# Optimization experiments

Hardware: AMD Instinct MI355X
Metric: run time of the kernel (lower is better)

The kernel has to match this reference:

```python
import jax, jax.numpy as jnp
import numpy as np

N_USERS = 100000
N_ITEMS = 50000
DIM = 64
NNZ_FULL = 3000000
NNZ_USER = 1500000
NNZ_ITEM = 750000


def setup_inputs() -> dict:
    key = jax.random.key(0)
    ks = jax.random.split(key, 11)
    N = N_USERS + N_ITEMS
    return {
        "user_emb": jax.random.normal(ks[0], (N_USERS, DIM), jnp.float32) * 0.1,
        "item_emb": jax.random.normal(ks[1], (N_ITEMS, DIM), jnp.float32) * 0.1,
        "full_rows": jax.random.randint(ks[2], (NNZ_FULL,), 0, N, jnp.int32),
        "full_cols": jax.random.randint(ks[3], (NNZ_FULL,), 0, N, jnp.int32),
        "full_vals": jax.random.uniform(ks[4], (NNZ_FULL,), jnp.float32),
        "user_rows": jax.random.randint(ks[5], (NNZ_USER,), 0, N_USERS, jnp.int32),
        "user_cols": jax.random.randint(ks[6], (NNZ_USER,), 0, N_USERS, jnp.int32),
        "user_vals": jax.random.uniform(ks[7], (NNZ_USER,), jnp.float32),
        "item_rows": jax.random.randint(ks[8], (NNZ_ITEM,), 0, N_ITEMS, jnp.int32),
        "item_cols": jax.random.randint(ks[9], (NNZ_ITEM,), 0, N_ITEMS, jnp.int32),
        "item_vals": jax.random.uniform(ks[10], (NNZ_ITEM,), jnp.float32),
    }


def _spmm(rows, cols, vals, x, n_rows):
    # COO sparse @ dense: gather columns, scale by edge value, scatter-add to rows.
    return jax.ops.segment_sum(vals[:, None] * x[cols], rows, num_segments=n_rows)


def reference(user_emb, item_emb,
              full_rows, full_cols, full_vals,
              user_rows, user_cols, user_vals,
              item_rows, item_cols, item_vals):
    n_u, n_i = user_emb.shape[0], item_emb.shape[0]
    all_emb = jnp.concatenate([user_emb, item_emb], axis=0)        # [(Nu+Ni), D]
    all_emb1 = _spmm(full_rows, full_cols, full_vals, all_emb, n_u + n_i)
    user_emb2 = _spmm(user_rows, user_cols, user_vals, user_emb, n_u)
    item_emb2 = _spmm(item_rows, item_cols, item_vals, item_emb, n_i)
    user_emb1, item_emb1 = all_emb1[:n_u], all_emb1[n_u:]
    return (user_emb1, item_emb1, user_emb2, item_emb2)
```

## Files before the change

kernel.cpp:

```cpp
#include <hip/hip_runtime.h>

#define NR_FULL 150000
#define NR_USER 100000
#define NR_ITEM 50000
#define NR_TOT  300000
#define NUSR    100000
#define NR_X    150000
#define DIM     64

#define BIN_ROWS  512
#define BIN_SHIFT 9
#define NBIN ((NR_TOT + BIN_ROWS - 1) / BIN_ROWS)

#define PART_E 8192
#define PART_T 512

#define SORT_T    512
#define SORT_CAP  12288
#define SORT2_CAP 5888

typedef __attribute__((ext_vector_type(4))) float f32x4;

__device__ __forceinline__ unsigned short f2bf(float f) {
    unsigned b = __float_as_uint(f);
    return (unsigned short)((b + 0x7fffu + ((b >> 16) & 1u)) >> 16);
}

__global__ void prep_kernel(const float* __restrict__ ue, const float* __restrict__ ie,
                            unsigned short* __restrict__ tbl,
                            const int* __restrict__ fr, int nf,
                            const int* __restrict__ ur, int nu,
                            const int* __restrict__ ir, int ni,
                            int* __restrict__ bincnt) {
    __shared__ int s_h[NBIN];
    for (int b = threadIdx.x; b < NBIN; b += blockDim.x) s_h[b] = 0;
    __syncthreads();

    int t = blockIdx.x * blockDim.x + threadIdx.x;
    int stride = gridDim.x * blockDim.x;

    const int nq = NR_X * (DIM / 4);
    for (int q = t; q < nq; q += stride) {
        int u  = q >> 4;
        int d4 = q & 15;
        const float* src = ((u < NUSR) ? ue + (size_t)u * DIM
                                       : ie + (size_t)(u - NUSR) * DIM) + d4 * 4;
        f32x4 f = *(const f32x4*)src;
        ushort4 h;
        h.x = f2bf(f.x); h.y = f2bf(f.y); h.z = f2bf(f.z); h.w = f2bf(f.w);
        ((ushort4*)tbl)[q] = h;
    }

    int nvec = nf >> 2;
    for (int i = t; i < nvec; i += stride) {
        int4 r4 = ((const int4*)fr)[i];
        atomicAdd(&s_h[r4.x >> BIN_SHIFT], 1);
        atomicAdd(&s_h[r4.y >> BIN_SHIFT], 1);
        atomicAdd(&s_h[r4.z >> BIN_SHIFT], 1);
        atomicAdd(&s_h[r4.w >> BIN_SHIFT], 1);
    }
    for (int i = (nvec << 2) + t; i < nf; i += stride)
        atomicAdd(&s_h[fr[i] >> BIN_SHIFT], 1);

    nvec = nu >> 2;
    for (int i = t; i < nvec; i += stride) {
        int4 r4 = ((const int4*)ur)[i];
        atomicAdd(&s_h[(r4.x + NR_FULL) >> BIN_SHIFT], 1);
        atomicAdd(&s_h[(r4.y + NR_FULL) >> BIN_SHIFT], 1);
        atomicAdd(&s_h[(r4.z + NR_FULL) >> BIN_SHIFT], 1);
        atomicAdd(&s_h[(r4.w + NR_FULL) >> BIN_SHIFT], 1);
    }
    for (int i = (nvec << 2) + t; i < nu; i += stride)
        atomicAdd(&s_h[(ur[i] + NR_FULL) >> BIN_SHIFT], 1);

    nvec = ni >> 2;
    for (int i = t; i < nvec; i += stride) {
        int4 r4 = ((const int4*)ir)[i];
        atomicAdd(&s_h[(r4.x + NR_FULL + NR_USER) >> BIN_SHIFT], 1);
        atomicAdd(&s_h[(r4.y + NR_FULL + NR_USER) >> BIN_SHIFT], 1);
        atomicAdd(&s_h[(r4.z + NR_FULL + NR_USER) >> BIN_SHIFT], 1);
        atomicAdd(&s_h[(r4.w + NR_FULL + NR_USER) >> BIN_SHIFT], 1);
    }
    for (int i = (nvec << 2) + t; i < ni; i += stride)
        atomicAdd(&s_h[(ir[i] + NR_FULL + NR_USER) >> BIN_SHIFT], 1);

    __syncthreads();
    for (int b = threadIdx.x; b < NBIN; b += blockDim.x) {
        int c = s_h[b];
        if (c) atomicAdd(&bincnt[b], c);
    }
}

__global__ void hist_all(const int* __restrict__ fr, int nf,
                         const int* __restrict__ ur, int nu,
                         const int* __restrict__ ir, int ni,
                         int* __restrict__ bincnt) {
    __shared__ int s_h[NBIN];
    for (int b = threadIdx.x; b < NBIN; b += blockDim.x) s_h[b] = 0;
    __syncthreads();
    int t = blockIdx.x * blockDim.x + threadIdx.x;
    int stride = gridDim.x * blockDim.x;
    int nvec = nf >> 2;
    for (int i = t; i < nvec; i += stride) {
        int4 r4 = ((const int4*)fr)[i];
        atomicAdd(&s_h[r4.x >> BIN_SHIFT], 1);
        atomicAdd(&s_h[r4.y >> BIN_SHIFT], 1);
        atomicAdd(&s_h[r4.z >> BIN_SHIFT], 1);
        atomicAdd(&s_h[r4.w >> BIN_SHIFT], 1);
    }
    for (int i = (nvec << 2) + t; i < nf; i += stride)
        atomicAdd(&s_h[fr[i] >> BIN_SHIFT], 1);
    nvec = nu >> 2;
    for (int i = t; i < nvec; i += stride) {
        int4 r4 = ((const int4*)ur)[i];
        atomicAdd(&s_h[(r4.x + NR_FULL) >> BIN_SHIFT], 1);
        atomicAdd(&s_h[(r4.y + NR_FULL) >> BIN_SHIFT], 1);
        atomicAdd(&s_h[(r4.z + NR_FULL) >> BIN_SHIFT], 1);
        atomicAdd(&s_h[(r4.w + NR_FULL) >> BIN_SHIFT], 1);
    }
    for (int i = (nvec << 2) + t; i < nu; i += stride)
        atomicAdd(&s_h[(ur[i] + NR_FULL) >> BIN_SHIFT], 1);
    nvec = ni >> 2;
    for (int i = t; i < nvec; i += stride) {
        int4 r4 = ((const int4*)ir)[i];
        atomicAdd(&s_h[(r4.x + NR_FULL + NR_USER) >> BIN_SHIFT], 1);
        atomicAdd(&s_h[(r4.y + NR_FULL + NR_USER) >> BIN_SHIFT], 1);
        atomicAdd(&s_h[(r4.z + NR_FULL + NR_USER) >> BIN_SHIFT], 1);
        atomicAdd(&s_h[(r4.w + NR_FULL + NR_USER) >> BIN_SHIFT], 1);
    }
    for (int i = (nvec << 2) + t; i < ni; i += stride)
        atomicAdd(&s_h[(ir[i] + NR_FULL + NR_USER) >> BIN_SHIFT], 1);
    __syncthreads();
    for (int b = threadIdx.x; b < NBIN; b += blockDim.x) {
        int c = s_h[b];
        if (c) atomicAdd(&bincnt[b], c);
    }
}

__global__ void bin_scan(const int* __restrict__ bincnt, int* __restrict__ binoff,
                         int* __restrict__ gcursor, int nnz_tot) {
    __shared__ int s[NBIN];
    int t = threadIdx.x;
    if (t < NBIN) s[t] = bincnt[t];
    __syncthreads();
    for (int off = 1; off < NBIN; off <<= 1) {
        int a = 0;
        if (t < NBIN && t >= off) a = s[t - off];
        __syncthreads();
        if (t < NBIN) s[t] += a;
        __syncthreads();
    }
    if (t < NBIN) {
        int excl = (t == 0) ? 0 : s[t - 1];
        binoff[t] = excl;
        gcursor[t] = excl;
    }
    if (t == 0) binoff[NBIN] = nnz_tot;
}

__global__ __launch_bounds__(PART_T) void partition_kernel(
    const int* __restrict__ fr, const int* __restrict__ fc, const float* __restrict__ fv, int nf,
    const int* __restrict__ ur, const int* __restrict__ uc, const float* __restrict__ uv, int nu,
    const int* __restrict__ ir, const int* __restrict__ ic, const float* __restrict__ iv, int ni,
    int* __restrict__ gcursor, long long* __restrict__ pairs) {
    __shared__ long long s_stage[PART_E];
    __shared__ int s_cnt[NBIN];
    __shared__ int s_start[NBIN + 1];
    __shared__ int s_cur[NBIN];
    __shared__ int s_gbase[NBIN];

    const int t = threadIdx.x;
    const int ntot = nf + nu + ni;
    const int base = blockIdx.x * PART_E;
    const int nE = min(PART_E, ntot - base);

    for (int b = t; b < NBIN; b += PART_T) s_cnt[b] = 0;
    __syncthreads();

    for (int k = 0; k < PART_E / PART_T; ++k) {
        int j = k * PART_T + t;
        if (j < nE) {
            int i = base + j;
            int g;
            if (i < nf)            g = fr[i];
            else if (i < nf + nu)  g = ur[i - nf] + NR_FULL;
            else                   g = ir[i - nf - nu] + NR_FULL + NR_USER;
            atomicAdd(&s_cnt[g >> BIN_SHIFT], 1);
        }
    }
    __syncthreads();

    for (int off = 1; off < NBIN; off <<= 1) {
        int i0 = t, i1 = t + PART_T;
        int a0 = (i0 < NBIN && i0 >= off) ? s_cnt[i0 - off] : 0;
        int a1 = (i1 < NBIN && i1 >= off) ? s_cnt[i1 - off] : 0;
        __syncthreads();
        if (i0 < NBIN) s_cnt[i0] += a0;
        if (i1 < NBIN) s_cnt[i1] += a1;
        __syncthreads();
    }
    for (int b = t; b < NBIN; b += PART_T) {
        int st = (b == 0) ? 0 : s_cnt[b - 1];
        s_start[b] = st;
        s_cur[b]   = st;
    }
    if (t == 0) s_start[NBIN] = s_cnt[NBIN - 1];
    __syncthreads();

    for (int b = t; b < NBIN; b += PART_T) {
        int cnt = s_start[b + 1] - s_start[b];
        s_gbase[b] = cnt ? atomicAdd(&gcursor[b], cnt) : 0;
    }

    for (int k = 0; k < PART_E / PART_T; ++k) {
        int j = k * PART_T + t;
        if (j < nE) {
            int i = base + j;
            int g, u; float v;
            if (i < nf)           { g = fr[i];                          u = fc[i];        v = fv[i]; }
            else if (i < nf + nu) { int q = i - nf;      g = ur[q] + NR_FULL;            u = uc[q];        v = uv[q]; }
            else                  { int q = i - nf - nu; g = ir[q] + NR_FULL + NR_USER;  u = ic[q] + NUSR; v = iv[q]; }
            int bin = g >> BIN_SHIFT;
            int rl  = g & (BIN_ROWS - 1);
            int lpos = atomicAdd(&s_cur[bin], 1);
            unsigned hi = ((unsigned)rl << 18) | (unsigned)u;
            s_stage[lpos] = ((long long)hi << 32) | (long long)__float_as_uint(v);
        }
    }
    __syncthreads();

    for (int j = t; j < nE; j += PART_T) {
        int lo = 0, hi2 = NBIN;
        while (hi2 - lo > 1) {
            int mid = (lo + hi2) >> 1;
            if (s_start[mid] <= j) lo = mid; else hi2 = mid;
        }
        pairs[s_gbase[lo] + (j - s_start[lo])] = s_stage[j];
    }
}

__global__ __launch_bounds__(SORT_T) void sort_bins_split(
    const int* __restrict__ binoff, const long long* __restrict__ pairs,
    long long* __restrict__ pairs2, int* __restrict__ rowptr, int nnz_tot) {
    __shared__ long long s_stage[SORT2_CAP];
    __shared__ int s_cnt[BIN_ROWS];
    __shared__ int s_start[BIN_ROWS];
    __shared__ int s_cur[BIN_ROWS];

    const int t    = threadIdx.x;
    const int bin  = blockIdx.x >> 1;
    const int half = blockIdx.x & 1;
    const int r0   = half * (BIN_ROWS / 2);
    const int r1   = r0 + (BIN_ROWS / 2);
    const int beg  = binoff[bin], end = binoff[bin + 1];
    const int nE   = end - beg;

    s_cnt[t] = 0;
    __syncthreads();

    const unsigned* hi32 = (const unsigned*)(pairs + beg) + 1;
    for (int j = t; j < nE; j += SORT_T)
        atomicAdd(&s_cnt[hi32[2 * j] >> 18], 1);
    __syncthreads();

    for (int off = 1; off < BIN_ROWS; off <<= 1) {
        int a = (t >= off) ? s_cnt[t - off] : 0;
        __syncthreads();
        s_cnt[t] += a;
        __syncthreads();
    }
    int excl = (t == 0) ? 0 : s_cnt[t - 1];
    s_start[t] = excl;
    s_cur[t]   = excl;
    if (t >= r0 && t < r1) {
        int g = bin * BIN_ROWS + t;
        if (g < NR_TOT) rowptr[g] = beg + excl;
    }
    if (bin == 0 && half == 0 && t == 0) rowptr[NR_TOT] = nnz_tot;
    __syncthreads();

    const int myBase  = s_start[r0];
    const int myCount = ((r1 < BIN_ROWS) ? s_start[r1] : s_cnt[BIN_ROWS - 1]) - myBase;
    const int nS = myCount < SORT2_CAP ? myCount : SORT2_CAP;

    for (int j = t; j < nE; j += SORT_T) {
        long long pe = pairs[beg + j];
        int rl = (int)((unsigned)((unsigned long long)pe >> 32) >> 18);
        if (rl >= r0 && rl < r1) {
            int pos = atomicAdd(&s_cur[rl], 1) - myBase;
            if (pos < SORT2_CAP) s_stage[pos] = pe;
        }
    }
    __syncthreads();

    for (int j = t; j < nS; j += SORT_T)
        pairs2[beg + myBase + j] = s_stage[j];
}

__global__ __launch_bounds__(SORT_T) void sort_bins(
    const int* __restrict__ binoff, long long* __restrict__ pairs,
    int* __restrict__ rowptr, int nnz_tot) {
    __shared__ long long s_stage[SORT_CAP];
    __shared__ int s_cnt[BIN_ROWS];
    __shared__ int s_start[BIN_ROWS];
    __shared__ int s_cur[BIN_ROWS];

    const int t   = threadIdx.x;
    const int bin = blockIdx.x;
    const int beg = binoff[bin], end = binoff[bin + 1];
    const int nE  = end - beg;
    const int nS  = nE < SORT_CAP ? nE : SORT_CAP;

    s_cnt[t] = 0;
    __syncthreads();
    for (int j = t; j < nE; j += SORT_T) {
        unsigned hi = (unsigned)((unsigned long long)pairs[beg + j] >> 32);
        atomicAdd(&s_cnt[hi >> 18], 1);
    }
    __syncthreads();
    for (int off = 1; off < BIN_ROWS; off <<= 1) {
        int a = (t >= off) ? s_cnt[t - off] : 0;
        __syncthreads();
        s_cnt[t] += a;
        __syncthreads();
    }
    int excl = (t == 0) ? 0 : s_cnt[t - 1];
    s_start[t] = excl;
    s_cur[t]   = excl;
    int g = bin * BIN_ROWS + t;
    if (g < NR_TOT) rowptr[g] = beg + excl;
    if (bin == 0 && t == 0) rowptr[NR_TOT] = nnz_tot;
    __syncthreads();
    for (int j = t; j < nE; j += SORT_T) {
        long long pe = pairs[beg + j];
        unsigned hi = (unsigned)((unsigned long long)pe >> 32);
        int pos = atomicAdd(&s_cur[hi >> 18], 1);
        if (pos < SORT_CAP) s_stage[pos] = pe;
    }
    __syncthreads();
    for (int j = t; j < nS; j += SORT_T)
        pairs[beg + j] = s_stage[j];
}

__global__ void spmm_bf16(const int* __restrict__ rowptr,
                          const long long* __restrict__ pairs,
                          const unsigned short* __restrict__ tbl,
                          float* __restrict__ out) {
    const int lane = threadIdx.x & 63;
    const int sub  = lane & 7;
    const int grp  = lane >> 3;
    int wave  = (blockIdx.x * blockDim.x + threadIdx.x) >> 6;
    int nwave = (gridDim.x * blockDim.x) >> 6;
    for (int g = wave; g < NR_TOT; g += nwave) {
        int beg = rowptr[g], end = rowptr[g + 1];
        float acc[8] = {0.f, 0.f, 0.f, 0.f, 0.f, 0.f, 0.f, 0.f};
        if (beg < end) {
            int elast = end - 1;
            for (int e0 = beg + grp * 2; e0 < end; e0 += 16) {
                float v[2];
                uint4 h[2];
#pragma unroll
                for (int i = 0; i < 2; ++i) {
                    int ee = e0 + i;
                    bool ok = ee < end;
                    ee = ok ? ee : elast;
                    long long p = __builtin_nontemporal_load(&pairs[ee]);
                    v[i] = ok ? __uint_as_float((unsigned)p) : 0.f;
                    unsigned u = ((unsigned)((unsigned long long)p >> 32)) & 0x3FFFF;
                    h[i] = ((const uint4*)(tbl + (size_t)u * DIM))[sub];
                }
#pragma unroll
                for (int i = 0; i < 2; ++i) {
                    acc[0] = fmaf(v[i], __uint_as_float(h[i].x << 16),         acc[0]);
                    acc[1] = fmaf(v[i], __uint_as_float(h[i].x & 0xffff0000u), acc[1]);
                    acc[2] = fmaf(v[i], __uint_as_float(h[i].y << 16),         acc[2]);
                    acc[3] = fmaf(v[i], __uint_as_float(h[i].y & 0xffff0000u), acc[3]);
                    acc[4] = fmaf(v[i], __uint_as_float(h[i].z << 16),         acc[4]);
                    acc[5] = fmaf(v[i], __uint_as_float(h[i].z & 0xffff0000u), acc[5]);
                    acc[6] = fmaf(v[i], __uint_as_float(h[i].w << 16),         acc[6]);
                    acc[7] = fmaf(v[i], __uint_as_float(h[i].w & 0xffff0000u), acc[7]);
                }
            }
#pragma unroll
            for (int k = 0; k < 8; ++k) {
                acc[k] += __shfl_xor(acc[k], 8);
                acc[k] += __shfl_xor(acc[k], 16);
                acc[k] += __shfl_xor(acc[k], 32);
            }
        }
        if (grp == 0) {
            f32x4 lo = {acc[0], acc[1], acc[2], acc[3]};
            f32x4 hi = {acc[4], acc[5], acc[6], acc[7]};
            f32x4* o = (f32x4*)(out + (size_t)g * DIM) + sub * 2;
            __builtin_nontemporal_store(lo, o);
            __builtin_nontemporal_store(hi, o + 1);
        }
    }
}

__global__ void spmm_rowreg(const int* __restrict__ rowptr,
                            const long long* __restrict__ pairs,
                            const float* __restrict__ user_emb,
                            const float* __restrict__ item_emb,
                            float* __restrict__ out) {
    const int lane = threadIdx.x & 63;
    const int sub  = lane & 15;
    const int grp  = lane >> 4;
    int wave  = (blockIdx.x * blockDim.x + threadIdx.x) >> 6;
    int nwave = (gridDim.x * blockDim.x) >> 6;
    for (int g = wave; g < NR_TOT; g += nwave) {
        int beg = rowptr[g], end = rowptr[g + 1];
        f32x4 acc = {0.f, 0.f, 0.f, 0.f};
        if (beg < end) {
            int elast = end - 1;
            for (int e = beg + grp; e < end; e += 8) {
                long long p0 = __builtin_nontemporal_load(&pairs[e]);
                int e1 = e + 4; bool ok1 = e1 <= elast; e1 = ok1 ? e1 : elast;
                long long p1 = __builtin_nontemporal_load(&pairs[e1]);
                float v0 = __uint_as_float((unsigned)p0);
                float v1 = ok1 ? __uint_as_float((unsigned)p1) : 0.f;
                unsigned u0 = ((unsigned)((unsigned long long)p0 >> 32)) & 0x3FFFF;
                unsigned u1 = ((unsigned)((unsigned long long)p1 >> 32)) & 0x3FFFF;
                const float* x0 = (u0 < NUSR) ? user_emb + (size_t)u0 * DIM
                                              : item_emb + (size_t)(u0 - NUSR) * DIM;
                const float* x1 = (u1 < NUSR) ? user_emb + (size_t)u1 * DIM
                                              : item_emb + (size_t)(u1 - NUSR) * DIM;
                f32x4 a = ((const f32x4*)x0)[sub];
                f32x4 b = ((const f32x4*)x1)[sub];
                acc.x = fmaf(v0, a.x, acc.x); acc.y = fmaf(v0, a.y, acc.y);
                acc.z = fmaf(v0, a.z, acc.z); acc.w = fmaf(v0, a.w, acc.w);
                acc.x = fmaf(v1, b.x, acc.x); acc.y = fmaf(v1, b.y, acc.y);
                acc.z = fmaf(v1, b.z, acc.z); acc.w = fmaf(v1, b.w, acc.w);
            }
            acc.x += __shfl_xor(acc.x, 16); acc.y += __shfl_xor(acc.y, 16);
            acc.z += __shfl_xor(acc.z, 16); acc.w += __shfl_xor(acc.w, 16);
            acc.x += __shfl_xor(acc.x, 32); acc.y += __shfl_xor(acc.y, 32);
            acc.z += __shfl_xor(acc.z, 32); acc.w += __shfl_xor(acc.w, 32);
        }
        if (grp == 0)
            __builtin_nontemporal_store(acc, (f32x4*)(out + (size_t)g * DIM) + sub);
    }
}

__global__ void spmm_scatter(const int* __restrict__ rows,
                             const int* __restrict__ cols,
                             const float* __restrict__ vals,
                             const float* __restrict__ emb_a,
                             const float* __restrict__ emb_b,
                             float* __restrict__ out,
                             int nnz, int split) {
    const int lane  = threadIdx.x & 63;
    const int wave  = (blockIdx.x * blockDim.x + threadIdx.x) >> 6;
    const int nwave = (gridDim.x * blockDim.x) >> 6;
    for (int e = wave; e < nnz; e += nwave) {
        const int   r = rows[e];
        const int   c = cols[e];
        const float v = vals[e];
        const float* xrow = (c < split) ? (emb_a + (size_t)c * DIM)
                                        : (emb_b + (size_t)(c - split) * DIM);
        unsafeAtomicAdd(out + (size_t)r * DIM + lane, v * xrow[lane]);
    }
}

extern "C" void kernel_launch(void* const* d_in, const int* in_sizes, int n_in,
                              void* d_out, int out_size, void* d_ws, size_t ws_size,
                              hipStream_t stream) {
    const float* user_emb  = (const float*)d_in[0];
    const float* item_emb  = (const float*)d_in[1];
    const int*   full_rows = (const int*)d_in[2];
    const int*   full_cols = (const int*)d_in[3];
    const float* full_vals = (const float*)d_in[4];
    const int*   user_rows = (const int*)d_in[5];
    const int*   user_cols = (const int*)d_in[6];
    const float* user_vals = (const float*)d_in[7];
    const int*   item_rows = (const int*)d_in[8];
    const int*   item_cols = (const int*)d_in[9];
    const float* item_vals = (const float*)d_in[10];

    float* out = (float*)d_out;

    const int nnz_full = in_sizes[2];
    const int nnz_user = in_sizes[5];
    const int nnz_item = in_sizes[8];
    const int nnz_tot  = nnz_full + nnz_user + nnz_item;

    size_t i_bincnt  = 0;
    size_t i_binoff  = i_bincnt + NBIN;
    size_t i_gcursor = i_binoff + NBIN + 1;
    size_t i_rowptr  = i_gcursor + NBIN;
    size_t i_end     = i_rowptr + NR_TOT + 1;
    i_end = (i_end + 3) & ~(size_t)3;
    size_t pairs_off   = i_end * sizeof(int);
    size_t pairs_bytes = (size_t)nnz_tot * sizeof(long long);
    size_t tbl_bytes   = (size_t)NR_X * DIM * sizeof(unsigned short);

    size_t after_pairs  = (pairs_off + pairs_bytes + 15) & ~(size_t)15;
    size_t pairs2_off   = after_pairs;
    size_t after_pairs2 = (pairs2_off + pairs_bytes + 15) & ~(size_t)15;

    size_t need_T3 = after_pairs2 + tbl_bytes;
    size_t need_T2 = after_pairs + tbl_bytes;
    size_t need_T1 = pairs_off + pairs_bytes;

    if (ws_size < need_T1) {
        float* all1  = out;
        float* user2 = out + (size_t)NR_FULL * DIM;
        float* item2 = user2 + (size_t)NR_USER * DIM;
        hipMemsetAsync(d_out, 0, (size_t)out_size * sizeof(float), stream);
        spmm_scatter<<<4096, 256, 0, stream>>>(full_rows, full_cols, full_vals,
                                               user_emb, item_emb, all1, nnz_full, NUSR);
        spmm_scatter<<<4096, 256, 0, stream>>>(user_rows, user_cols, user_vals,
                                               user_emb, user_emb, user2, nnz_user, 0x7fffffff);
        spmm_scatter<<<4096, 256, 0, stream>>>(item_rows, item_cols, item_vals,
                                               item_emb, item_emb, item2, nnz_item, 0x7fffffff);
        return;
    }

    const bool split_sort = (ws_size >= need_T3);
    const bool use_bf16   = (ws_size >= need_T2);

    int*            ws_i    = (int*)d_ws;
    int*            bincnt  = ws_i + i_bincnt;
    int*            binoff  = ws_i + i_binoff;
    int*            gcursor = ws_i + i_gcursor;
    int*            rowptr  = ws_i + i_rowptr;
    long long*      pairs   = (long long*)((char*)d_ws + pairs_off);
    long long*      pairs2  = (long long*)((char*)d_ws + pairs2_off);
    unsigned short* tbl     = (unsigned short*)((char*)d_ws +
                                  (split_sort ? after_pairs2 : after_pairs));

    hipMemsetAsync(bincnt, 0, NBIN * sizeof(int), stream);

    if (use_bf16)
        prep_kernel<<<1024, 256, 0, stream>>>(user_emb, item_emb, tbl,
                                              full_rows, nnz_full,
                                              user_rows, nnz_user,
                                              item_rows, nnz_item, bincnt);
    else
        hist_all<<<768, 256, 0, stream>>>(full_rows, nnz_full,
                                          user_rows, nnz_user,
                                          item_rows, nnz_item, bincnt);

    bin_scan<<<1, 1024, 0, stream>>>(bincnt, binoff, gcursor, nnz_tot);

    const int nchunk = (nnz_tot + PART_E - 1) / PART_E;
    partition_kernel<<<nchunk, PART_T, 0, stream>>>(
        full_rows, full_cols, full_vals, nnz_full,
        user_rows, user_cols, user_vals, nnz_user,
        item_rows, item_cols, item_vals, nnz_item,
        gcursor, pairs);

    const long long* sorted;
    if (split_sort) {
        sort_bins_split<<<NBIN * 2, SORT_T, 0, stream>>>(binoff, pairs, pairs2,
                                                         rowptr, nnz_tot);
        sorted = pairs2;
    } else {
        sort_bins<<<NBIN, SORT_T, 0, stream>>>(binoff, pairs, rowptr, nnz_tot);
        sorted = pairs;
    }

    if (use_bf16)
        spmm_bf16<<<4096, 256, 0, stream>>>(rowptr, sorted, tbl, out);
    else
        spmm_rowreg<<<4096, 256, 0, stream>>>(rowptr, sorted, user_emb, item_emb, out);
}
```

Baseline: 264.4 us.

## Replace split bin sort with single-block sort using wave-shuffle scan and direct scatter

The per-bin counting sort no longer splits each bin across two blocks. The Hillis-Steele shared-memory scan with many barriers becomes a wave-level shuffle scan plus a small cross-wave fixup, and the LDS staging buffer is dropped so elements scatter straight to global memory at their sorted position. This cuts barrier count, LDS use and the duplicated histogram pass, at the cost of uncoalesced global writes and half as many blocks.

```diff
diff --git a/kernel.cpp b/kernel.cpp
--- a/kernel.cpp
+++ b/kernel.cpp
@@ -15,9 +15,8 @@
 #define PART_E 8192
 #define PART_T 512
 
-#define SORT_T    512
-#define SORT_CAP  12288
-#define SORT2_CAP 5888
+#define SORT_T   512
+#define SORT_CAP 12288
 
 typedef __attribute__((ext_vector_type(4))) float f32x4;
 
@@ -239,21 +238,17 @@
     }
 }
 
-__global__ __launch_bounds__(SORT_T) void sort_bins_split(
+__global__ __launch_bounds__(SORT_T) void sort_bins_v2(
     const int* __restrict__ binoff, const long long* __restrict__ pairs,
     long long* __restrict__ pairs2, int* __restrict__ rowptr, int nnz_tot) {
-    __shared__ long long s_stage[SORT2_CAP];
     __shared__ int s_cnt[BIN_ROWS];
-    __shared__ int s_start[BIN_ROWS];
     __shared__ int s_cur[BIN_ROWS];
-
-    const int t    = threadIdx.x;
-    const int bin  = blockIdx.x >> 1;
-    const int half = blockIdx.x & 1;
-    const int r0   = half * (BIN_ROWS / 2);
-    const int r1   = r0 + (BIN_ROWS / 2);
-    const int beg  = binoff[bin], end = binoff[bin + 1];
-    const int nE   = end - beg;
+    __shared__ int s_wsum[SORT_T / 64];
+
+    const int t   = threadIdx.x;
+    const int bin = blockIdx.x;
+    const int beg = binoff[bin], end = binoff[bin + 1];
+    const int nE  = end - beg;
 
     s_cnt[t] = 0;
     __syncthreads();
@@ -263,38 +258,36 @@
         atomicAdd(&s_cnt[hi32[2 * j] >> 18], 1);
     __syncthreads();
 
-    for (int off = 1; off < BIN_ROWS; off <<= 1) {
-        int a = (t >= off) ? s_cnt[t - off] : 0;
-        __syncthreads();
-        s_cnt[t] += a;
-        __syncthreads();
-    }
-    int excl = (t == 0) ? 0 : s_cnt[t - 1];
-    s_start[t] = excl;
-    s_cur[t]   = excl;
-    if (t >= r0 && t < r1) {
-        int g = bin * BIN_ROWS + t;
-        if (g < NR_TOT) rowptr[g] = beg + excl;
-    }
-    if (bin == 0 && half == 0 && t == 0) rowptr[NR_TOT] = nnz_tot;
-    __syncthreads();
-
-    const int myBase  = s_start[r0];
-    const int myCount = ((r1 < BIN_ROWS) ? s_start[r1] : s_cnt[BIN_ROWS - 1]) - myBase;
-    const int nS = myCount < SORT2_CAP ? myCount : SORT2_CAP;
+    const int lane = t & 63, wid = t >> 6;
+    int cnt0 = s_cnt[t];
+    int x = cnt0;
+    #pragma unroll
+    for (int off = 1; off < 64; off <<= 1) {
+        int y = __shfl_up(x, off);
+        if (lane >= off) x += y;
+    }
+    if (lane == 63) s_wsum[wid] = x;
+    __syncthreads();
+    if (t == 0) {
+        int run = 0;
+        #pragma unroll
+        for (int w = 0; w < SORT_T / 64; ++w) { int c = s_wsum[w]; s_wsum[w] = run; run += c; }
+    }
+    __syncthreads();
+    int excl = x + s_wsum[wid] - cnt0;
+
+    s_cur[t] = excl;
+    int g = bin * BIN_ROWS + t;
+    if (g < NR_TOT) rowptr[g] = beg + excl;
+    if (bin == 0 && t == 0) rowptr[NR_TOT] = nnz_tot;
+    __syncthreads();
 
     for (int j = t; j < nE; j += SORT_T) {
         long long pe = pairs[beg + j];
         int rl = (int)((unsigned)((unsigned long long)pe >> 32) >> 18);
-        if (rl >= r0 && rl < r1) {
-            int pos = atomicAdd(&s_cur[rl], 1) - myBase;
-            if (pos < SORT2_CAP) s_stage[pos] = pe;
-        }
-    }
-    __syncthreads();
-
-    for (int j = t; j < nS; j += SORT_T)
-        pairs2[beg + myBase + j] = s_stage[j];
+        int pos = atomicAdd(&s_cur[rl], 1);
+        pairs2[beg + pos] = pe;
+    }
 }
 
 __global__ __launch_bounds__(SORT_T) void sort_bins(
@@ -516,8 +509,8 @@
         return;
     }
 
-    const bool split_sort = (ws_size >= need_T3);
-    const bool use_bf16   = (ws_size >= need_T2);
+    const bool v2_sort  = (ws_size >= need_T3);
+    const bool use_bf16 = (ws_size >= need_T2);
 
     int*            ws_i    = (int*)d_ws;
     int*            bincnt  = ws_i + i_bincnt;
@@ -527,7 +520,7 @@
     long long*      pairs   = (long long*)((char*)d_ws + pairs_off);
     long long*      pairs2  = (long long*)((char*)d_ws + pairs2_off);
     unsigned short* tbl     = (unsigned short*)((char*)d_ws +
-                                  (split_sort ? after_pairs2 : after_pairs));
+                                  (v2_sort ? after_pairs2 : after_pairs));
 
     hipMemsetAsync(bincnt, 0, NBIN * sizeof(int), stream);
 
@@ -551,9 +544,9 @@
         gcursor, pairs);
 
     const long long* sorted;
-    if (split_sort) {
-        sort_bins_split<<<NBIN * 2, SORT_T, 0, stream>>>(binoff, pairs, pairs2,
-                                                         rowptr, nnz_tot);
+    if (v2_sort) {
+        sort_bins_v2<<<NBIN, SORT_T, 0, stream>>>(binoff, pairs, pairs2,
+                                                  rowptr, nnz_tot);
         sorted = pairs2;
     } else {
         sort_bins<<<NBIN, SORT_T, 0, stream>>>(binoff, pairs, rowptr, nnz_tot);
```

After: 289.0 us. 9.3% more time.
